# Optimization experiments

Hardware: AMD Instinct MI355X
Metric: run time of the kernel (lower is better)

The kernel has to match this reference:

```python
import jax, jax.numpy as jnp
import numpy as np

NUM_SAMPLED = 8192
NUM_TRUE = 1


def setup_inputs() -> dict:
    key = jax.random.key(0)
    k1, k2, k3 = jax.random.split(key, 3)
    B, D, V = 16384, 128, 1000000
    return {
        "movie_id_tensor": jax.random.normal(k1, (B, D), dtype=jnp.float32),
        "target_movie_ids": jax.random.randint(k2, (B, NUM_TRUE), 0, V, dtype=jnp.int64),
        "embedding": jax.random.normal(k3, (V, D), dtype=jnp.float32),
        "bias": jnp.zeros((V,), dtype=jnp.float32),
    }


def _log_uniform_logprob(ids, log_range):
    # log-uniform (Zipf) sampler probability: P(c) = (log(c+2)-log(c+1)) / log(V+1)
    idsf = ids.astype(jnp.float32)
    return jnp.log((jnp.log(idsf + 2.0) - jnp.log(idsf + 1.0)) / log_range)


def reference(movie_id_tensor, target_movie_ids, embedding, bias):
    V, D = embedding.shape
    log_range = jnp.log(jnp.float32(V + 1))
    # --- draw num_sampled candidates from the log-uniform distribution ---
    u = jax.random.uniform(jax.random.key(1), (NUM_SAMPLED,), dtype=jnp.float32)
    sampled = jnp.clip(
        jnp.floor(jnp.exp(u * log_range)).astype(jnp.int32) - 1, 0, V - 1
    )  # [S]
    log_ns = jnp.log(jnp.float32(NUM_SAMPLED))
    # --- gather true-class rows and compute true logits (with logQ correction) ---
    true_w = embedding[target_movie_ids]                  # [B, T, D]
    true_b = bias[target_movie_ids]                       # [B, T]
    true_logits = (
        jnp.einsum("bd,btd->bt", movie_id_tensor, true_w)
        + true_b
        - (log_ns + _log_uniform_logprob(target_movie_ids, log_range))
    )                                                     # [B, T]
    # --- sampled logits (shared candidate set across the batch) ---
    sampled_w = embedding[sampled]                        # [S, D]
    sampled_b = bias[sampled]                             # [S]
    sampled_logits = (
        movie_id_tensor @ sampled_w.T
        + sampled_b
        - (log_ns + _log_uniform_logprob(sampled, log_range))
    )                                                     # [B, S]
    # --- remove accidental hits (sampled id equals a true label) ---
    hit = (sampled[None, None, :] == target_movie_ids[:, :, None]).any(axis=1)  # [B, S]
    sampled_logits = jnp.where(hit, sampled_logits - 1e9, sampled_logits)
    # --- softmax CE with labels = 1/num_true on the true columns ---
    logits = jnp.concatenate([true_logits, sampled_logits], axis=1)  # [B, T+S]
    loss = jax.nn.logsumexp(logits, axis=1) - true_logits.sum(axis=1) / NUM_TRUE
    return loss  # [B]
```

## Files before the change

kernel.cpp:

```cpp
#include <hip/hip_runtime.h>
#include <math.h>

#define BB      16384
#define DD      128
#define VV      1000000
#define NSAMP   8192
#define NT      (NSAMP / 64)

typedef __attribute__((ext_vector_type(8)))  unsigned short u16x8;
typedef __attribute__((ext_vector_type(8)))  __bf16         bf16x8;
typedef __attribute__((ext_vector_type(16))) float          f32x16;

__device__ __forceinline__ unsigned rotl32(unsigned x, unsigned r) {
    return (x << r) | (x >> (32u - r));
}

__device__ __forceinline__ unsigned short bf16r(float v) {
    unsigned b = __builtin_bit_cast(unsigned, v);
    unsigned r = (b + 0x7fffu + ((b >> 16) & 1u)) >> 16;
    return (unsigned short)r;
}

__device__ __forceinline__ void gload16(const void* g, void* l) {
    __builtin_amdgcn_global_load_lds(
        (const __attribute__((address_space(1))) unsigned*)g,
        (__attribute__((address_space(3))) unsigned*)l, 16, 0, 0);
}

__device__ __forceinline__ float xla_expf(float x) {
#pragma clang fp contract(off)
    float fx = floorf(x * 1.44269504088896341f + 0.5f);
    float tmp = fx * 0.693359375f;
    float z2  = fx * -2.12194440e-4f;
    float r = x - tmp;
    r = r - z2;
    float z = r * r;
    float y = 1.9875691500E-4f;
    y = y * r + 1.3981999507E-3f;
    y = y * r + 8.3334519073E-3f;
    y = y * r + 4.1665795894E-2f;
    y = y * r + 1.6666665459E-1f;
    y = y * r + 5.0000001201E-1f;
    y = y * z + r;
    y = y + 1.0f;
    int n = (int)fx;
    float p2n = __builtin_bit_cast(float, (unsigned)((n + 127) << 23));
    return y * p2n;
}

__device__ __forceinline__ float log_q32(float idf, float logr) {
    float l2 = (float)log((double)(idf + 2.0f));
    float l1 = (float)log((double)(idf + 1.0f));
    float q  = (l2 - l1) / logr;
    return (float)log((double)q);
}

__global__ __launch_bounds__(256) void prep_kernel(
    const float* __restrict__ x, const unsigned* __restrict__ tgt_raw,
    const float* __restrict__ bias,
    unsigned short* __restrict__ Xb,
    int* __restrict__ ids, float* __restrict__ corr,
    unsigned* __restrict__ flag, float logr, float logns)
{
    if (blockIdx.x == 0) {
        __shared__ unsigned red[256];
        unsigned acc = 0;
        for (int i = threadIdx.x; i < 2048; i += 256) acc |= tgt_raw[2 * i + 1];
        red[threadIdx.x] = acc;
        __syncthreads();
        for (int s = 128; s > 0; s >>= 1) {
            if ((int)threadIdx.x < s) red[threadIdx.x] |= red[threadIdx.x + s];
            __syncthreads();
        }
        if (threadIdx.x == 0) flag[0] = (red[0] == 0u) ? 1u : 0u;
    }

    int g = blockIdx.x * 256 + threadIdx.x;
    {
        int row = g >> 4, chunk = g & 15;
        const float4* src = (const float4*)(x + (size_t)row * DD + chunk * 8);
        float4 a = src[0], b = src[1];
        uint4 o;
        o.x = (unsigned)bf16r(a.x) | ((unsigned)bf16r(a.y) << 16);
        o.y = (unsigned)bf16r(a.z) | ((unsigned)bf16r(a.w) << 16);
        o.z = (unsigned)bf16r(b.x) | ((unsigned)bf16r(b.y) << 16);
        o.w = (unsigned)bf16r(b.z) | ((unsigned)bf16r(b.w) << 16);
        *(uint4*)(Xb + (size_t)row * DD + chunk * 8) = o;
    }

    if (g < NSAMP) {
        int i = g;
        const unsigned k0 = 0u, k1 = 1u;
        const unsigned k2 = 0x1BD11BDAu ^ k0 ^ k1;
        unsigned x0 = 0u + k0;
        unsigned x1 = (unsigned)i + k1;
#define TFR(r) { x0 += x1; x1 = rotl32(x1, (r)); x1 ^= x0; }
        TFR(13) TFR(15) TFR(26) TFR(6)   x0 += k1; x1 += k2 + 1u;
        TFR(17) TFR(29) TFR(16) TFR(24)  x0 += k2; x1 += k0 + 2u;
        TFR(13) TFR(15) TFR(26) TFR(6)   x0 += k0; x1 += k1 + 3u;
        TFR(17) TFR(29) TFR(16) TFR(24)  x0 += k1; x1 += k2 + 4u;
        TFR(13) TFR(15) TFR(26) TFR(6)   x0 += k2; x1 += k0 + 5u;
#undef TFR
        unsigned bits = x0 ^ x1;

        unsigned fb = (bits >> 9) | 0x3f800000u;
        float u = __builtin_bit_cast(float, fb) - 1.0f;
        float t = u * logr;
        float ef = xla_expf(t);
        int id = (int)floorf(ef) - 1;
        id = id < 0 ? 0 : (id > VV - 1 ? VV - 1 : id);

        float lp = log_q32((float)id, logr);
        ids[i]  = id;
        corr[i] = bias[id] - (logns + lp);
    }
}

__global__ __launch_bounds__(256) void gather_kernel(
    const float* __restrict__ emb, const int* __restrict__ ids,
    unsigned short* __restrict__ Wh)
{
    int g = blockIdx.x * 256 + threadIdx.x;
    int row   = g >> 4;
    int chunk = g & 15;
    const float4* src = (const float4*)(emb + (size_t)ids[row] * DD + chunk * 8);
    float4 a = src[0], b = src[1];
    uint4 o;
    o.x = (unsigned)bf16r(a.x) | ((unsigned)bf16r(a.y) << 16);
    o.y = (unsigned)bf16r(a.z) | ((unsigned)bf16r(a.w) << 16);
    o.z = (unsigned)bf16r(b.x) | ((unsigned)bf16r(b.y) << 16);
    o.w = (unsigned)bf16r(b.z) | ((unsigned)bf16r(b.w) << 16);
    *(uint4*)(Wh + (size_t)row * DD + chunk * 8) = o;
}

__device__ __forceinline__ int swz(int row, int slot) {
    return row * 256 + ((slot ^ (row & 15)) << 4);
}

__global__ __launch_bounds__(256, 2) void gemm_kernel(
    const unsigned short* __restrict__ Xb, const int* __restrict__ tgt,
    const unsigned* __restrict__ flag,
    const unsigned short* __restrict__ Wh,
    const int* __restrict__ ids, const float* __restrict__ corr,
    float* __restrict__ ps)
{
    __shared__ char lds[32768];

    const int tid  = threadIdx.x;
    const int lane = tid & 63;
    const int wid  = tid >> 6;
    const int wr   = wid >> 1, wc = wid & 1;
    const int half = lane >> 5, ln31 = lane & 31;
    const int m0   = blockIdx.x * 128;
    const int ty0  = blockIdx.y * (NT / 4);

    u16x8 ah[2][8];
    #pragma unroll
    for (int p = 0; p < 2; p++) {
        const uint4* xr = (const uint4*)(Xb + (size_t)(m0 + wr * 64 + p * 32 + ln31) * DD);
        #pragma unroll
        for (int ks = 0; ks < 8; ks++)
            ah[p][ks] = __builtin_bit_cast(u16x8, xr[ks * 2 + half]);
    }

    const unsigned is64 = flag[0];
    int t32[2][16];
    #pragma unroll
    for (int p = 0; p < 2; p++)
        #pragma unroll
        for (int i = 0; i < 16; i++) {
            int grow = m0 + wr * 64 + p * 32 + (i & 3) + 8 * (i >> 2) + 4 * half;
            t32[p][i] = is64 ? tgt[2 * grow] : tgt[grow];
        }

    float ss[2][16];
    #pragma unroll
    for (int p = 0; p < 2; p++)
        #pragma unroll
        for (int i = 0; i < 16; i++) ss[p][i] = 0.f;

    const int u    = lane & 15;
    const int rsub = lane >> 4;
    int srcoff[4], ldsrow[4];
    #pragma unroll
    for (int i2 = 0; i2 < 4; i2++) {
        int row = wid * 16 + i2 * 4 + rsub;
        srcoff[i2] = row * 256 + ((u ^ (row & 15)) << 4);
        ldsrow[i2] = (wid * 16 + i2 * 4) * 256;
    }
    const int brow = wc * 32 + ln31;

    {
        const char* tb = (const char*)Wh + (size_t)(ty0 * 64) * 256;
        #pragma unroll
        for (int i2 = 0; i2 < 4; i2++)
            gload16(tb + srcoff[i2], lds + ldsrow[i2]);
    }
    __syncthreads();

    for (int t = 0; t < NT / 4; t++) {
        const int c = t & 1;
        if (t + 1 < NT / 4) {
            const char* tb = (const char*)Wh + (size_t)((ty0 + t + 1) * 64) * 256;
            char* db = lds + (c ^ 1) * 16384;
            #pragma unroll
            for (int i2 = 0; i2 < 4; i2++)
                gload16(tb + srcoff[i2], db + ldsrow[i2]);
        }

        const char* bh_base = lds + c * 16384;
        f32x16 h0, h1;
        #pragma unroll
        for (int q = 0; q < 16; q++) { h0[q] = 0.f; h1[q] = 0.f; }

        #pragma unroll
        for (int ks = 0; ks < 8; ks++) {
            int off = swz(brow, ks * 2 + half);
            bf16x8 bh = __builtin_bit_cast(bf16x8, *(const uint4*)(bh_base + off));
            bf16x8 a0 = __builtin_bit_cast(bf16x8, ah[0][ks]);
            bf16x8 a1 = __builtin_bit_cast(bf16x8, ah[1][ks]);
            h0 = __builtin_amdgcn_mfma_f32_32x32x16_bf16(a0, bh, h0, 0, 0, 0);
            h1 = __builtin_amdgcn_mfma_f32_32x32x16_bf16(a1, bh, h1, 0, 0, 0);
        }

        const int j = (ty0 + t) * 64 + wc * 32 + ln31;
        const float cc = corr[j] - 60.0f;
        const int idj = ids[j];
        #pragma unroll
        for (int i = 0; i < 16; i++) {
            float l0 = h0[i] + cc;
            float l1 = h1[i] + cc;
            ss[0][i] += (idj == t32[0][i]) ? 0.0f : __expf(l0);
            ss[1][i] += (idj == t32[1][i]) ? 0.0f : __expf(l1);
        }

        __syncthreads();
    }

    #pragma unroll
    for (int p = 0; p < 2; p++)
        #pragma unroll
        for (int i = 0; i < 16; i++) {
            float v = ss[p][i];
            v += __shfl_xor(v, 1);
            v += __shfl_xor(v, 2);
            v += __shfl_xor(v, 4);
            v += __shfl_xor(v, 8);
            v += __shfl_xor(v, 16);
            if (ln31 == 0) {
                int grow = m0 + wr * 64 + p * 32 + (i & 3) + 8 * (i >> 2) + 4 * half;
                ps[(size_t)grow * 8 + blockIdx.y * 2 + wc] = v;
            }
        }
}

__global__ __launch_bounds__(256) void finish_kernel(
    const float* __restrict__ x, const int* __restrict__ tgt,
    const float* __restrict__ emb, const float* __restrict__ bias,
    const unsigned* __restrict__ flag, const float* __restrict__ ps,
    float* __restrict__ out, float logr, float logns)
{
    const int gid = blockIdx.x * 256 + threadIdx.x;
    const int r   = gid >> 4;
    const int l   = gid & 15;
    if (r >= BB) return;

    const int t = flag[0] ? tgt[2 * r] : tgt[r];

    const float4* xr = (const float4*)(x + (size_t)r * DD);
    const float4* wr = (const float4*)(emb + (size_t)t * DD);
    float4 xa = xr[l], xb = xr[l + 16];
    float4 wa = wr[l], wb = wr[l + 16];
    float d = xa.x*wa.x + xa.y*wa.y + xa.z*wa.z + xa.w*wa.w
            + xb.x*wb.x + xb.y*wb.y + xb.z*wb.z + xb.w*wb.w;
    d += __shfl_xor(d, 1);
    d += __shfl_xor(d, 2);
    d += __shfl_xor(d, 4);
    d += __shfl_xor(d, 8);

    if (l == 0) {
        float lp = log_q32((float)t, logr);
        float tl = d + bias[t] - (logns + lp);
        const float* p = ps + (size_t)r * 8;
        float S = ((p[0] + p[1]) + (p[2] + p[3])) + ((p[4] + p[5]) + (p[6] + p[7]));
        out[r] = logf(expf(tl - 60.0f) + S) + 60.0f - tl;
    }
}

extern "C" void kernel_launch(void* const* d_in, const int* in_sizes, int n_in,
                              void* d_out, int out_size, void* d_ws, size_t ws_size,
                              hipStream_t stream)
{
    const float* x    = (const float*)d_in[0];
    const int*   tgt  = (const int*)d_in[1];
    const float* emb  = (const float*)d_in[2];
    const float* bias = (const float*)d_in[3];
    float* out = (float*)d_out;

    char* w = (char*)d_ws;
    int*            ids  = (int*)(w + 0);
    float*          corr = (float*)(w + 32768);
    unsigned*       flag = (unsigned*)(w + 65536);
    unsigned short* Xb   = (unsigned short*)(w + 131072);
    unsigned short* Wh   = (unsigned short*)(w + 131072 + 4194304);
    float*          ps   = (float*)(w + 131072 + 4194304 + 2097152);

    const float logr  = (float)log(1000001.0);
    const float logns = (float)log(8192.0);

    prep_kernel<<<dim3(BB * 16 / 256), dim3(256), 0, stream>>>(
        x, (const unsigned*)tgt, bias, Xb, ids, corr, flag, logr, logns);
    gather_kernel<<<dim3(NSAMP * 16 / 256), dim3(256), 0, stream>>>(
        emb, ids, Wh);
    gemm_kernel<<<dim3(BB / 128, 4), dim3(256), 0, stream>>>(
        Xb, tgt, flag, Wh, ids, corr, ps);
    finish_kernel<<<dim3(BB * 16 / 256), dim3(256), 0, stream>>>(
        x, tgt, emb, bias, flag, ps, out, logr, logns);
}
```

Before: 75.05 us.

## Keep sampled-weight fragments in registers and stream batch rows through GEMM

```diff
diff --git a/kernel.cpp b/kernel.cpp
--- a/kernel.cpp
+++ b/kernel.cpp
@@ -5,7 +5,6 @@
 #define DD      128
 #define VV      1000000
 #define NSAMP   8192
-#define NT      (NSAMP / 64)
 
 typedef __attribute__((ext_vector_type(8)))  unsigned short u16x8;
 typedef __attribute__((ext_vector_type(8)))  __bf16         bf16x8;
@@ -19,12 +18,6 @@
     unsigned b = __builtin_bit_cast(unsigned, v);
     unsigned r = (b + 0x7fffu + ((b >> 16) & 1u)) >> 16;
     return (unsigned short)r;
-}
-
-__device__ __forceinline__ void gload16(const void* g, void* l) {
-    __builtin_amdgcn_global_load_lds(
-        (const __attribute__((address_space(1))) unsigned*)g,
-        (__attribute__((address_space(3))) unsigned*)l, 16, 0, 0);
 }
 
 __device__ __forceinline__ float xla_expf(float x) {
@@ -133,10 +126,6 @@
     *(uint4*)(Wh + (size_t)row * DD + chunk * 8) = o;
 }
 
-__device__ __forceinline__ int swz(int row, int slot) {
-    return row * 256 + ((slot ^ (row & 15)) << 4);
-}
-
 __global__ __launch_bounds__(256, 2) void gemm_kernel(
     const unsigned short* __restrict__ Xb, const int* __restrict__ tgt,
     const unsigned* __restrict__ flag,
@@ -144,114 +133,73 @@
     const int* __restrict__ ids, const float* __restrict__ corr,
     float* __restrict__ ps)
 {
-    __shared__ char lds[32768];
-
     const int tid  = threadIdx.x;
     const int lane = tid & 63;
     const int wid  = tid >> 6;
-    const int wr   = wid >> 1, wc = wid & 1;
     const int half = lane >> 5, ln31 = lane & 31;
-    const int m0   = blockIdx.x * 128;
-    const int ty0  = blockIdx.y * (NT / 4);
-
-    u16x8 ah[2][8];
+    const int cb   = blockIdx.x;
+    const int r0   = blockIdx.y * 1024;
+    const int cw   = cb * 256 + wid * 64;
+
+    u16x8 wf[2][8];
     #pragma unroll
-    for (int p = 0; p < 2; p++) {
-        const uint4* xr = (const uint4*)(Xb + (size_t)(m0 + wr * 64 + p * 32 + ln31) * DD);
+    for (int g = 0; g < 2; g++) {
+        const uint4* wr_ = (const uint4*)(Wh + (size_t)(cw + g * 32 + ln31) * DD);
         #pragma unroll
         for (int ks = 0; ks < 8; ks++)
-            ah[p][ks] = __builtin_bit_cast(u16x8, xr[ks * 2 + half]);
-    }
+            wf[g][ks] = __builtin_bit_cast(u16x8, wr_[ks * 2 + half]);
+    }
+
+    int   idv[2][16];
+    float cv[2][16];
+    #pragma unroll
+    for (int g = 0; g < 2; g++)
+        #pragma unroll
+        for (int i = 0; i < 16; i++) {
+            int j = cw + g * 32 + (i & 3) + 8 * (i >> 2) + 4 * half;
+            idv[g][i] = ids[j];
+            cv[g][i]  = corr[j] - 60.0f;
+        }
 
     const unsigned is64 = flag[0];
-    int t32[2][16];
-    #pragma unroll
-    for (int p = 0; p < 2; p++)
+    float* psw = ps + (size_t)(cb * 4 + wid) * BB + r0;
+
+    for (int it = 0; it < 32; it++) {
+        const int m = r0 + it * 32;
+
+        const uint4* xr = (const uint4*)(Xb + (size_t)(m + ln31) * DD);
+        u16x8 bx[8];
+        #pragma unroll
+        for (int ks = 0; ks < 8; ks++)
+            bx[ks] = __builtin_bit_cast(u16x8, xr[ks * 2 + half]);
+
+        const int trow = m + ln31;
+        const int t_lane = is64 ? tgt[2 * trow] : tgt[trow];
+
+        f32x16 a0, a1;
+        #pragma unroll
+        for (int q = 0; q < 16; q++) { a0[q] = 0.f; a1[q] = 0.f; }
+
+        #pragma unroll
+        for (int ks = 0; ks < 8; ks++) {
+            bf16x8 b  = __builtin_bit_cast(bf16x8, bx[ks]);
+            bf16x8 w0 = __builtin_bit_cast(bf16x8, wf[0][ks]);
+            bf16x8 w1 = __builtin_bit_cast(bf16x8, wf[1][ks]);
+            a0 = __builtin_amdgcn_mfma_f32_32x32x16_bf16(w0, b, a0, 0, 0, 0);
+            a1 = __builtin_amdgcn_mfma_f32_32x32x16_bf16(w1, b, a1, 0, 0, 0);
+        }
+
+        float s = 0.f;
         #pragma unroll
         for (int i = 0; i < 16; i++) {
-            int grow = m0 + wr * 64 + p * 32 + (i & 3) + 8 * (i >> 2) + 4 * half;
-            t32[p][i] = is64 ? tgt[2 * grow] : tgt[grow];
-        }
-
-    float ss[2][16];
-    #pragma unroll
-    for (int p = 0; p < 2; p++)
-        #pragma unroll
-        for (int i = 0; i < 16; i++) ss[p][i] = 0.f;
-
-    const int u    = lane & 15;
-    const int rsub = lane >> 4;
-    int srcoff[4], ldsrow[4];
-    #pragma unroll
-    for (int i2 = 0; i2 < 4; i2++) {
-        int row = wid * 16 + i2 * 4 + rsub;
-        srcoff[i2] = row * 256 + ((u ^ (row & 15)) << 4);
-        ldsrow[i2] = (wid * 16 + i2 * 4) * 256;
-    }
-    const int brow = wc * 32 + ln31;
-
-    {
-        const char* tb = (const char*)Wh + (size_t)(ty0 * 64) * 256;
-        #pragma unroll
-        for (int i2 = 0; i2 < 4; i2++)
-            gload16(tb + srcoff[i2], lds + ldsrow[i2]);
-    }
-    __syncthreads();
-
-    for (int t = 0; t < NT / 4; t++) {
-        const int c = t & 1;
-        if (t + 1 < NT / 4) {
-            const char* tb = (const char*)Wh + (size_t)((ty0 + t + 1) * 64) * 256;
-            char* db = lds + (c ^ 1) * 16384;
-            #pragma unroll
-            for (int i2 = 0; i2 < 4; i2++)
-                gload16(tb + srcoff[i2], db + ldsrow[i2]);
-        }
-
-        const char* bh_base = lds + c * 16384;
-        f32x16 h0, h1;
-        #pragma unroll
-        for (int q = 0; q < 16; q++) { h0[q] = 0.f; h1[q] = 0.f; }
-
-        #pragma unroll
-        for (int ks = 0; ks < 8; ks++) {
-            int off = swz(brow, ks * 2 + half);
-            bf16x8 bh = __builtin_bit_cast(bf16x8, *(const uint4*)(bh_base + off));
-            bf16x8 a0 = __builtin_bit_cast(bf16x8, ah[0][ks]);
-            bf16x8 a1 = __builtin_bit_cast(bf16x8, ah[1][ks]);
-            h0 = __builtin_amdgcn_mfma_f32_32x32x16_bf16(a0, bh, h0, 0, 0, 0);
-            h1 = __builtin_amdgcn_mfma_f32_32x32x16_bf16(a1, bh, h1, 0, 0, 0);
-        }
-
-        const int j = (ty0 + t) * 64 + wc * 32 + ln31;
-        const float cc = corr[j] - 60.0f;
-        const int idj = ids[j];
-        #pragma unroll
-        for (int i = 0; i < 16; i++) {
-            float l0 = h0[i] + cc;
-            float l1 = h1[i] + cc;
-            ss[0][i] += (idj == t32[0][i]) ? 0.0f : __expf(l0);
-            ss[1][i] += (idj == t32[1][i]) ? 0.0f : __expf(l1);
-        }
-
-        __syncthreads();
-    }
-
-    #pragma unroll
-    for (int p = 0; p < 2; p++)
-        #pragma unroll
-        for (int i = 0; i < 16; i++) {
-            float v = ss[p][i];
-            v += __shfl_xor(v, 1);
-            v += __shfl_xor(v, 2);
-            v += __shfl_xor(v, 4);
-            v += __shfl_xor(v, 8);
-            v += __shfl_xor(v, 16);
-            if (ln31 == 0) {
-                int grow = m0 + wr * 64 + p * 32 + (i & 3) + 8 * (i >> 2) + 4 * half;
-                ps[(size_t)grow * 8 + blockIdx.y * 2 + wc] = v;
-            }
-        }
+            float l0 = a0[i] + cv[0][i];
+            float l1 = a1[i] + cv[1][i];
+            s += (idv[0][i] == t_lane) ? 0.0f : __expf(l0);
+            s += (idv[1][i] == t_lane) ? 0.0f : __expf(l1);
+        }
+        s += __shfl_xor(s, 32);
+        if (half == 0) psw[it * 32 + ln31] = s;
+    }
 }
 
 __global__ __launch_bounds__(256) void finish_kernel(
@@ -260,31 +208,34 @@
     const unsigned* __restrict__ flag, const float* __restrict__ ps,
     float* __restrict__ out, float logr, float logns)
 {
-    const int gid = blockIdx.x * 256 + threadIdx.x;
-    const int r   = gid >> 4;
-    const int l   = gid & 15;
+    int r = blockIdx.x * 256 + threadIdx.x;
     if (r >= BB) return;
-
-    const int t = flag[0] ? tgt[2 * r] : tgt[r];
+    int t = flag[0] ? tgt[2 * r] : tgt[r];
 
     const float4* xr = (const float4*)(x + (size_t)r * DD);
     const float4* wr = (const float4*)(emb + (size_t)t * DD);
-    float4 xa = xr[l], xb = xr[l + 16];
-    float4 wa = wr[l], wb = wr[l + 16];
-    float d = xa.x*wa.x + xa.y*wa.y + xa.z*wa.z + xa.w*wa.w
-            + xb.x*wb.x + xb.y*wb.y + xb.z*wb.z + xb.w*wb.w;
-    d += __shfl_xor(d, 1);
-    d += __shfl_xor(d, 2);
-    d += __shfl_xor(d, 4);
-    d += __shfl_xor(d, 8);
-
-    if (l == 0) {
-        float lp = log_q32((float)t, logr);
-        float tl = d + bias[t] - (logns + lp);
-        const float* p = ps + (size_t)r * 8;
-        float S = ((p[0] + p[1]) + (p[2] + p[3])) + ((p[4] + p[5]) + (p[6] + p[7]));
-        out[r] = logf(expf(tl - 60.0f) + S) + 60.0f - tl;
-    }
+    float a0 = 0.f, a1 = 0.f, a2 = 0.f, a3 = 0.f;
+    #pragma unroll
+    for (int k = 0; k < 32; k += 4) {
+        float4 xv0 = xr[k],   wv0 = wr[k];
+        float4 xv1 = xr[k+1], wv1 = wr[k+1];
+        float4 xv2 = xr[k+2], wv2 = wr[k+2];
+        float4 xv3 = xr[k+3], wv3 = wr[k+3];
+        a0 += xv0.x*wv0.x + xv0.y*wv0.y + xv0.z*wv0.z + xv0.w*wv0.w;
+        a1 += xv1.x*wv1.x + xv1.y*wv1.y + xv1.z*wv1.z + xv1.w*wv1.w;
+        a2 += xv2.x*wv2.x + xv2.y*wv2.y + xv2.z*wv2.z + xv2.w*wv2.w;
+        a3 += xv3.x*wv3.x + xv3.y*wv3.y + xv3.z*wv3.z + xv3.w*wv3.w;
+    }
+    float dot = (a0 + a1) + (a2 + a3);
+    float lp  = log_q32((float)t, logr);
+    float tl  = dot + bias[t] - (logns + lp);
+
+    float S = 0.f;
+    #pragma unroll 8
+    for (int cb = 0; cb < 128; cb++)
+        S += ps[(size_t)cb * BB + r];
+
+    out[r] = logf(expf(tl - 60.0f) + S) + 60.0f - tl;
 }
 
 extern "C" void kernel_launch(void* const* d_in, const int* in_sizes, int n_in,
@@ -312,8 +263,8 @@
         x, (const unsigned*)tgt, bias, Xb, ids, corr, flag, logr, logns);
     gather_kernel<<<dim3(NSAMP * 16 / 256), dim3(256), 0, stream>>>(
         emb, ids, Wh);
-    gemm_kernel<<<dim3(BB / 128, 4), dim3(256), 0, stream>>>(
+    gemm_kernel<<<dim3(32, 16), dim3(256), 0, stream>>>(
         Xb, tgt, flag, Wh, ids, corr, ps);
-    finish_kernel<<<dim3(BB * 16 / 256), dim3(256), 0, stream>>>(
+    finish_kernel<<<dim3(BB / 256), dim3(256), 0, stream>>>(
         x, tgt, emb, bias, flag, ps, out, logr, logns);
 }
```

Result: slower. 122.1 us (+62.6%).

## Triple-buffer LDS tiles with prefetch distance two and a single barrier

Applied to the files above, without the earlier changes.

```diff
diff --git a/kernel.cpp b/kernel.cpp
--- a/kernel.cpp
+++ b/kernel.cpp
@@ -144,7 +144,7 @@
     const int* __restrict__ ids, const float* __restrict__ corr,
     float* __restrict__ ps)
 {
-    __shared__ char lds[32768];
+    __shared__ char lds[49152];
 
     const int tid  = threadIdx.x;
     const int lane = tid & 63;
@@ -153,6 +153,7 @@
     const int half = lane >> 5, ln31 = lane & 31;
     const int m0   = blockIdx.x * 128;
     const int ty0  = blockIdx.y * (NT / 4);
+    const int NTB  = NT / 4;
 
     u16x8 ah[2][8];
     #pragma unroll
@@ -191,24 +192,33 @@
     const int brow = wc * 32 + ln31;
 
     {
-        const char* tb = (const char*)Wh + (size_t)(ty0 * 64) * 256;
-        #pragma unroll
-        for (int i2 = 0; i2 < 4; i2++)
-            gload16(tb + srcoff[i2], lds + ldsrow[i2]);
-    }
-    __syncthreads();
-
-    for (int t = 0; t < NT / 4; t++) {
-        const int c = t & 1;
-        if (t + 1 < NT / 4) {
-            const char* tb = (const char*)Wh + (size_t)((ty0 + t + 1) * 64) * 256;
-            char* db = lds + (c ^ 1) * 16384;
+        const char* tb0 = (const char*)Wh + (size_t)(ty0 * 64) * 256;
+        const char* tb1 = (const char*)Wh + (size_t)((ty0 + 1) * 64) * 256;
+        #pragma unroll
+        for (int i2 = 0; i2 < 4; i2++) gload16(tb0 + srcoff[i2], lds + ldsrow[i2]);
+        #pragma unroll
+        for (int i2 = 0; i2 < 4; i2++) gload16(tb1 + srcoff[i2], lds + 16384 + ldsrow[i2]);
+    }
+
+    for (int t = 0; t < NTB; t++) {
+        asm volatile("s_waitcnt vmcnt(4)" ::: "memory");
+        __builtin_amdgcn_sched_barrier(0);
+        __builtin_amdgcn_s_barrier();
+
+        const int j = (ty0 + t) * 64 + wc * 32 + ln31;
+        const float cc = corr[j] - 60.0f;
+        const int idj = ids[j];
+        __builtin_amdgcn_sched_barrier(0);
+
+        {
+            int tn = t + 2 < NTB ? t + 2 : NTB - 1;
+            const char* tb = (const char*)Wh + (size_t)((ty0 + tn) * 64) * 256;
+            char* db = lds + ((t + 2) % 3) * 16384;
             #pragma unroll
-            for (int i2 = 0; i2 < 4; i2++)
-                gload16(tb + srcoff[i2], db + ldsrow[i2]);
-        }
-
-        const char* bh_base = lds + c * 16384;
+            for (int i2 = 0; i2 < 4; i2++) gload16(tb + srcoff[i2], db + ldsrow[i2]);
+        }
+
+        const char* bh_base = lds + (t % 3) * 16384;
         f32x16 h0, h1;
         #pragma unroll
         for (int q = 0; q < 16; q++) { h0[q] = 0.f; h1[q] = 0.f; }
@@ -223,9 +233,6 @@
             h1 = __builtin_amdgcn_mfma_f32_32x32x16_bf16(a1, bh, h1, 0, 0, 0);
         }
 
-        const int j = (ty0 + t) * 64 + wc * 32 + ln31;
-        const float cc = corr[j] - 60.0f;
-        const int idj = ids[j];
         #pragma unroll
         for (int i = 0; i < 16; i++) {
             float l0 = h0[i] + cc;
@@ -233,8 +240,6 @@
             ss[0][i] += (idj == t32[0][i]) ? 0.0f : __expf(l0);
             ss[1][i] += (idj == t32[1][i]) ? 0.0f : __expf(l1);
         }
-
-        __syncthreads();
     }
 
     #pragma unroll
```

Result: slower. 77.63 us (+3.4%).

## Software-pipeline MFMA compute with the exp epilogue of the previous tile

Applied to the files above, without the earlier changes.

```diff
diff --git a/kernel.cpp b/kernel.cpp
--- a/kernel.cpp
+++ b/kernel.cpp
@@ -153,6 +153,7 @@
     const int half = lane >> 5, ln31 = lane & 31;
     const int m0   = blockIdx.x * 128;
     const int ty0  = blockIdx.y * (NT / 4);
+    const int NTB  = NT / 4;
 
     u16x8 ah[2][8];
     #pragma unroll
@@ -190,29 +191,17 @@
     }
     const int brow = wc * 32 + ln31;
 
-    {
-        const char* tb = (const char*)Wh + (size_t)(ty0 * 64) * 256;
+    auto dma = [&](int tt, int buf) {
+        const char* tb = (const char*)Wh + (size_t)((ty0 + tt) * 64) * 256;
+        char* db = lds + buf * 16384;
         #pragma unroll
         for (int i2 = 0; i2 < 4; i2++)
-            gload16(tb + srcoff[i2], lds + ldsrow[i2]);
-    }
-    __syncthreads();
-
-    for (int t = 0; t < NT / 4; t++) {
-        const int c = t & 1;
-        if (t + 1 < NT / 4) {
-            const char* tb = (const char*)Wh + (size_t)((ty0 + t + 1) * 64) * 256;
-            char* db = lds + (c ^ 1) * 16384;
-            #pragma unroll
-            for (int i2 = 0; i2 < 4; i2++)
-                gload16(tb + srcoff[i2], db + ldsrow[i2]);
-        }
-
-        const char* bh_base = lds + c * 16384;
-        f32x16 h0, h1;
+            gload16(tb + srcoff[i2], db + ldsrow[i2]);
+    };
+    auto comp = [&](int tt, f32x16& h0, f32x16& h1) {
+        const char* bh_base = lds + (tt & 1) * 16384;
         #pragma unroll
         for (int q = 0; q < 16; q++) { h0[q] = 0.f; h1[q] = 0.f; }
-
         #pragma unroll
         for (int ks = 0; ks < 8; ks++) {
             int off = swz(brow, ks * 2 + half);
@@ -222,20 +211,36 @@
             h0 = __builtin_amdgcn_mfma_f32_32x32x16_bf16(a0, bh, h0, 0, 0, 0);
             h1 = __builtin_amdgcn_mfma_f32_32x32x16_bf16(a1, bh, h1, 0, 0, 0);
         }
-
-        const int j = (ty0 + t) * 64 + wc * 32 + ln31;
+    };
+    auto epi = [&](int tt, const f32x16& e0, const f32x16& e1) {
+        const int j = (ty0 + tt) * 64 + wc * 32 + ln31;
         const float cc = corr[j] - 60.0f;
         const int idj = ids[j];
         #pragma unroll
         for (int i = 0; i < 16; i++) {
-            float l0 = h0[i] + cc;
-            float l1 = h1[i] + cc;
+            float l0 = e0[i] + cc;
+            float l1 = e1[i] + cc;
             ss[0][i] += (idj == t32[0][i]) ? 0.0f : __expf(l0);
             ss[1][i] += (idj == t32[1][i]) ? 0.0f : __expf(l1);
         }
-
+    };
+
+    dma(0, 0);
+    __syncthreads();
+
+    f32x16 hA0, hA1, hB0, hB1;
+    for (int t = 0; t < NTB; t += 2) {
+        if (t + 1 < NTB) dma(t + 1, 1);
+        comp(t, hA0, hA1);
+        if (t > 0) epi(t - 1, hB0, hB1);
         __syncthreads();
-    }
+
+        if (t + 2 < NTB) dma(t + 2, 0);
+        comp(t + 1, hB0, hB1);
+        epi(t, hA0, hA1);
+        __syncthreads();
+    }
+    epi(NTB - 1, hB0, hB1);
 
     #pragma unroll
     for (int p = 0; p < 2; p++)
```

Measured after the change: 81.60 us. +8.7%, slower.
